# Kernel optimization log

Measured on AMD Instinct MI355X. Metric: run time of the kernel, lower is better.

The kernel has to match this reference:

```python
import jax, jax.numpy as jnp
import numpy as np

D_MODEL, D_STATE, D_CONV, EXPAND, N_HEADS = 768, 64, 4, 2, 12
D_INNER = D_MODEL * EXPAND           # 1536
HEAD_DIM = D_INNER // N_HEADS        # 128
IN_PROJ = D_INNER * 2 + N_HEADS * D_STATE * 2 + N_HEADS  # 4620
EPS = 1e-5


def setup_inputs() -> dict:
    key = jax.random.key(0)
    ks = jax.random.split(key, 8)
    s = lambda fan_in: 1.0 / np.sqrt(fan_in)
    return {
        "x": jax.random.normal(ks[0], (1, 1024, D_MODEL), dtype=jnp.float32),
        "W_in": jax.random.normal(ks[1], (IN_PROJ, D_MODEL), dtype=jnp.float32) * s(D_MODEL),
        "conv_w": jax.random.normal(ks[2], (D_INNER, D_CONV), dtype=jnp.float32) * s(D_CONV),
        "conv_b": jnp.zeros((D_INNER,), dtype=jnp.float32),
        "A_log": jnp.full((N_HEADS,), np.log(0.5), dtype=jnp.float32),
        "Dp": jnp.ones((N_HEADS,), dtype=jnp.float32),
        "dt_bias": jnp.zeros((N_HEADS,), dtype=jnp.float32),
        "W_out": jax.random.normal(ks[3], (D_MODEL, D_INNER), dtype=jnp.float32) * s(D_INNER),
        "norm_w": jnp.ones((D_INNER,), dtype=jnp.float32),
    }


def _causal_conv1d(x, w, b):
    # x: (B,L,Din), depthwise causal conv with kernel size D_CONV
    L = x.shape[1]
    xp = jnp.pad(x, ((0, 0), (D_CONV - 1, 0), (0, 0)))
    y = b
    for i in range(D_CONV):  # fixed small kernel, unrolled
        y = y + xp[:, i:i + L, :] * w[:, i]
    return y


def reference(x, W_in, conv_w, conv_b, A_log, Dp, dt_bias, W_out, norm_w):
    B_sz, L, _ = x.shape
    nh, ds, hd = N_HEADS, D_STATE, HEAD_DIM
    proj = jnp.einsum('bld,pd->blp', x, W_in)
    z = proj[:, :, :D_INNER]
    x_ssm = proj[:, :, D_INNER:2 * D_INNER]
    o = 2 * D_INNER
    Bm = proj[:, :, o:o + nh * ds].reshape(B_sz, L, nh, ds)
    Cm = proj[:, :, o + nh * ds:o + 2 * nh * ds].reshape(B_sz, L, nh, ds)
    dt_r = proj[:, :, o + 2 * nh * ds:]
    dt = jax.nn.softplus(dt_r) + dt_bias[None, None, :]          # (B,L,nh)

    x_ssm = jax.nn.silu(_causal_conv1d(x_ssm, conv_w, conv_b))
    x_ssm = x_ssm.reshape(B_sz, L, nh, hd)

    A = -jnp.exp(A_log)                                          # (nh,)
    log_decay = A[None, None, :] * dt                            # (B,L,nh)
    Phi = jnp.cumsum(log_decay, axis=1)
    dB = dt[..., None] * Bm                                      # (B,L,nh,ds)
    # b: (B,L,nh,hd,ds) outer product
    b = dB[:, :, :, None, :] * x_ssm[..., None]
    max_exp = 80.0
    exp_neg_Phi = jnp.exp(jnp.minimum(-Phi, max_exp))[..., None, None]
    b_cumsum = jnp.cumsum(exp_neg_Phi * b, axis=1)
    h = jnp.exp(Phi)[..., None, None] * b_cumsum                 # (B,L,nh,hd,ds)
    y = jnp.sum(Cm[:, :, :, None, :] * h, axis=-1)               # (B,L,nh,hd)
    y = y + Dp[None, None, :, None] * x_ssm
    y = y.reshape(B_sz, L, D_INNER)

    # RMSNorm then gate
    rms = jax.lax.rsqrt(jnp.mean(y * y, axis=-1, keepdims=True) + EPS)
    y = y * rms * norm_w
    y = y * jax.nn.silu(z)
    return jnp.einsum('bli,di->bld', y, W_out)
```

## Files before the change

### kernel.cpp

```cpp
#include <hip/hip_runtime.h>
#include <cmath>

#define LSEQ   1024
#define NPROJ  4620
#define NPADW  4736
#define DINNER 1536
#define NH     12
#define HDIM   128
#define OFF_Z  0
#define OFF_X  1536
#define OFF_B  3072
#define OFF_C  3840
#define OFF_DT 4608

typedef unsigned short u16;
typedef unsigned int u32;
typedef short bf16x8 __attribute__((ext_vector_type(8)));
typedef float f32x4 __attribute__((ext_vector_type(4)));

__device__ inline u16 f2b(float f) {
  unsigned u = __float_as_uint(f);
  return (u16)((u + 0x7fffu + ((u >> 16) & 1u)) >> 16);
}
__device__ inline float b2f(u16 h) { return __uint_as_float(((unsigned)h) << 16); }
__device__ inline u32 pk2(float a, float b) { return (u32)f2b(a) | ((u32)f2b(b) << 16); }

__device__ inline void gll16(const void* g, void* l) {
  __builtin_amdgcn_global_load_lds((const __attribute__((address_space(1))) void*)g,
                                   (__attribute__((address_space(3))) void*)l, 16, 0, 0);
}

#define S0N 196608
#define S1N 909312
#define S1V 887040
#define S2N 294912
__global__ __launch_bounds__(256) void ksplit_all(const float* __restrict__ x,
    const float* __restrict__ Wi, const float* __restrict__ Wo,
    u16* __restrict__ Ah, u16* __restrict__ Wh, u16* __restrict__ Woh) {
  int i = blockIdx.x * 256 + threadIdx.x;
  const float* src; u16* hi; int j, valid;
  if (i < S0N)            { src = x;  hi = Ah;  j = i;              valid = S0N; }
  else if (i < S0N + S1N) { src = Wi; hi = Wh;  j = i - S0N;        valid = S1V; }
  else                    { src = Wo; hi = Woh; j = i - S0N - S1N;  valid = S2N; }
  float4 v = (j < valid) ? ((const float4*)src)[j] : make_float4(0.f, 0.f, 0.f, 0.f);
  ((uint2*)hi)[j] = make_uint2(pk2(v.x, v.y), pk2(v.z, v.w));
}

template<int BM, int BN, int MAP, bool NG>
__global__ __launch_bounds__(256) void gemm1(const u16* __restrict__ Ah,
    const u16* __restrict__ Wh, float* __restrict__ C,
    int lda, int ldw, int Ksl, int Nreal, int ldc) {
  constexpr int PLA = BM * 64;
  constexpr int IA = BM / 8, IW = BN / 8, ITOT = IA + IW;
  constexpr int FRn = BN / 32;
  __shared__ u16 lds[PLA + BN * 64];
  const int tid = threadIdx.x;
  const int l = tid & 63, w = tid >> 6;
  const int wm = w >> 1, wn = w & 1;
  const int kg = l >> 4, li = l & 15;

  int b = blockIdx.x, m0, n0, koff;
  float* Cp = C;
  if (MAP == 0) {
    int xcd = b & 7, idx = b >> 3;
    m0 = (idx & 15) * 64;
    n0 = (xcd * 5 + (idx >> 4)) * 128;
    koff = 0;
    if (NG && n0 >= NPADW) return;
  } else {
    int xcd = b & 7, idx = b >> 3;
    int gg = xcd * 6 + (idx >> 4);
    m0 = (idx & 15) * 64;
    n0 = (gg % 12) * 64;
    koff = (gg / 12) * 384;
    Cp = C + (size_t)(gg / 12) * LSEQ * ldc;
  }

  const int srcg = ((l & 7) ^ (l >> 3)) * 8;
  auto stage = [&](int t) {
    const int k0 = koff + t * 64;
    for (int q = w; q < ITOT; q += 4) {
      const u16* gb; int r0b, ldk, dst;
      if (q < IA) { gb = Ah; r0b = m0 + 8 * q;        dst = 8 * q * 64;              ldk = lda; }
      else        { gb = Wh; r0b = n0 + 8 * (q - IA); dst = PLA + 8 * (q - IA) * 64; ldk = ldw; }
      gll16(gb + (size_t)(r0b + (l >> 3)) * ldk + k0 + srcg, &lds[dst]);
    }
  };
  auto rd = [&](int region, int row, int ks) -> bf16x8 {
    return *(const bf16x8*)&lds[region + row * 64 + (((ks * 4 + kg) ^ (row & 7)) << 3)];
  };

  f32x4 acc[2][FRn];
#pragma unroll
  for (int m = 0; m < 2; ++m)
#pragma unroll
    for (int n = 0; n < FRn; ++n) acc[m][n] = (f32x4){0.f, 0.f, 0.f, 0.f};

  const int NT = Ksl / 64;
  stage(0);
  asm volatile("s_waitcnt vmcnt(0)" ::: "memory");
  __syncthreads();
  for (int t = 0; t < NT; ++t) {
    bf16x8 af[2][2], wf[FRn][2];
#pragma unroll
    for (int ks = 0; ks < 2; ++ks) {
#pragma unroll
      for (int m = 0; m < 2; ++m)
        af[m][ks] = rd(0, wm * 32 + m * 16 + li, ks);
#pragma unroll
      for (int n = 0; n < FRn; ++n)
        wf[n][ks] = rd(PLA, wn * (BN / 2) + n * 16 + li, ks);
    }
    __syncthreads();
    if (t + 1 < NT) stage(t + 1);
#pragma unroll
    for (int ks = 0; ks < 2; ++ks)
#pragma unroll
      for (int m = 0; m < 2; ++m)
#pragma unroll
        for (int n = 0; n < FRn; ++n)
          acc[m][n] = __builtin_amdgcn_mfma_f32_16x16x32_bf16(af[m][ks], wf[n][ks], acc[m][n], 0, 0, 0);
    if (t + 1 < NT) {
      asm volatile("s_waitcnt vmcnt(0)" ::: "memory");
      __syncthreads();
    }
  }
#pragma unroll
  for (int m = 0; m < 2; ++m) {
    int rbase = m0 + wm * 32 + m * 16 + kg * 4;
#pragma unroll
    for (int n = 0; n < FRn; ++n) {
      int col = n0 + wn * (BN / 2) + n * 16 + li;
      if (!NG || col < Nreal) {
#pragma unroll
        for (int r = 0; r < 4; ++r)
          Cp[(size_t)(rbase + r) * ldc + col] = acc[m][n][r];
      }
    }
  }
}

__global__ __launch_bounds__(256) void addk(const float* __restrict__ P,
    float* __restrict__ out) {
  const int S = LSEQ * 768 / 4;
  int i = blockIdx.x * 256 + threadIdx.x;
  float4 a = ((const float4*)P)[i];
  float4 b = ((const float4*)P)[i + S];
  float4 c = ((const float4*)P)[i + 2 * S];
  float4 d = ((const float4*)P)[i + 3 * S];
  ((float4*)out)[i] = make_float4(a.x + b.x + c.x + d.x, a.y + b.y + c.y + d.y,
                                  a.z + b.z + c.z + d.z, a.w + b.w + c.w + d.w);
}

__global__ __launch_bounds__(256) void dtphi(const float* __restrict__ proj,
    const float* __restrict__ A_log, const float* __restrict__ dt_bias,
    float* __restrict__ Phi, float* __restrict__ dts) {
  int h = blockIdx.x, tid = threadIdx.x;
  float Ac = -expf(A_log[h]);
  float bb = dt_bias[h];
  float v[4], s = 0.f;
#pragma unroll
  for (int u = 0; u < 4; ++u) {
    int t = tid * 4 + u;
    float xr = proj[(size_t)t * NPROJ + OFF_DT + h];
    float sp = (xr > 20.f) ? xr : log1pf(expf(xr));
    v[u] = sp + bb;
    s += v[u];
  }
  int lane = tid & 63, wv = tid >> 6;
  float ps = s;
#pragma unroll
  for (int d = 1; d < 64; d <<= 1) {
    float o = __shfl_up(ps, d);
    if (lane >= d) ps += o;
  }
  __shared__ float wsum[4];
  if (lane == 63) wsum[wv] = ps;
  __syncthreads();
  float off = 0.f;
  for (int w = 0; w < wv; ++w) off += wsum[w];
  float run = off + ps - s;
#pragma unroll
  for (int u = 0; u < 4; ++u) {
    int t = tid * 4 + u;
    run += v[u];
    Phi[t * NH + h] = Ac * run;
    dts[t * NH + h] = v[u];
  }
}

__global__ __launch_bounds__(256) void conv_state(const float* __restrict__ proj,
    const float* __restrict__ cw, const float* __restrict__ cb,
    const float* __restrict__ Phi, const float* __restrict__ dts,
    u16* __restrict__ xactT, float* __restrict__ SlocF) {
  const int k = blockIdx.x, h = blockIdx.y, tid = threadIdx.x;
  const int l = tid & 63, w = tid >> 6, kg = l >> 4, li = l & 15;
  __shared__ u16 Bw[64 * 64];
  __shared__ u16 Xt[128 * 64];
  __shared__ float wS[64];
  const int s0 = k * 64;
  if (tid < 64) {
    float pe = Phi[(s0 + 63) * NH + h];
    float p  = Phi[(s0 + tid) * NH + h];
    wS[tid] = expf(pe + fminf(-p, 80.f)) * dts[(s0 + tid) * NH + h];
  }
  __syncthreads();
#pragma unroll
  for (int u = 0; u < 4; ++u) {
    int idx = tid + u * 256, s = idx >> 4, q = (idx & 15) * 4;
    float4 v = *(const float4*)(proj + (size_t)(s0 + s) * NPROJ + OFF_B + h * 64 + q);
    float ws_ = wS[s];
    float vv[4] = {v.x, v.y, v.z, v.w};
#pragma unroll
    for (int j = 0; j < 4; ++j) {
      int d = q + j;
      Bw[d * 64 + (((s >> 3) ^ (d & 7)) << 3) + (s & 7)] = f2b(vv[j] * ws_);
    }
  }
  {
    int c = tid & 127, th = tid >> 7;
    int cg = h * HDIM + c;
    float w0 = cw[cg * 4], w1 = cw[cg * 4 + 1], w2 = cw[cg * 4 + 2], w3 = cw[cg * 4 + 3];
    float bias = cb[cg];
    int tb = s0 + th * 32;
    auto P = [&](int t) { return (t >= 0) ? proj[(size_t)t * NPROJ + OFF_X + cg] : 0.f; };
    float x0 = P(tb - 3), x1 = P(tb - 2), x2 = P(tb - 1);
    u32 pkb[16];
    float prev = 0.f;
#pragma unroll
    for (int i = 0; i < 32; ++i) {
      float x3 = P(tb + i);
      float a = bias;
      a = fmaf(x0, w0, a); a = fmaf(x1, w1, a); a = fmaf(x2, w2, a); a = fmaf(x3, w3, a);
      float sv = a / (1.f + expf(-a));
      if (i & 1) pkb[i >> 1] = pk2(prev, sv); else prev = sv;
      x0 = x1; x1 = x2; x2 = x3;
    }
#pragma unroll
    for (int g = 0; g < 4; ++g) {
      int sg = th * 4 + g;
      *(uint4*)&Xt[c * 64 + ((sg ^ (c & 7)) << 3)] =
          make_uint4(pkb[g * 4], pkb[g * 4 + 1], pkb[g * 4 + 2], pkb[g * 4 + 3]);
    }
    size_t xo = ((size_t)(k * NH + h) * 128 + c) * 64 + th * 32;
#pragma unroll
    for (int g = 0; g < 4; ++g)
      *(uint4*)(xactT + xo + g * 8) =
          make_uint4(pkb[g * 4], pkb[g * 4 + 1], pkb[g * 4 + 2], pkb[g * 4 + 3]);
  }
  __syncthreads();
  const int wm = w >> 1, wn = w & 1;
  auto rd = [&](const u16* reg, int row, int ks) -> bf16x8 {
    return *(const bf16x8*)&reg[row * 64 + (((ks * 4 + kg) ^ (row & 7)) << 3)];
  };
  f32x4 acc[4][2];
#pragma unroll
  for (int m = 0; m < 4; ++m)
#pragma unroll
    for (int n = 0; n < 2; ++n) acc[m][n] = (f32x4){0.f, 0.f, 0.f, 0.f};
#pragma unroll
  for (int ks = 0; ks < 2; ++ks) {
    bf16x8 xf[4], bf[2];
#pragma unroll
    for (int m = 0; m < 4; ++m) xf[m] = rd(Xt, wm * 64 + m * 16 + li, ks);
#pragma unroll
    for (int n = 0; n < 2; ++n) bf[n] = rd(Bw, wn * 32 + n * 16 + li, ks);
#pragma unroll
    for (int m = 0; m < 4; ++m)
#pragma unroll
      for (int n = 0; n < 2; ++n)
        acc[m][n] = __builtin_amdgcn_mfma_f32_16x16x32_bf16(xf[m], bf[n], acc[m][n], 0, 0, 0);
  }
  float* dst = SlocF + ((size_t)(k * NH + h) << 13);
#pragma unroll
  for (int m = 0; m < 4; ++m)
#pragma unroll
    for (int n = 0; n < 2; ++n)
#pragma unroll
      for (int r = 0; r < 4; ++r) {
        int c = wm * 64 + m * 16 + kg * 4 + r;
        int d = wn * 32 + n * 16 + li;
        dst[c * 64 + d] = acc[m][n][r];
      }
}

__global__ __launch_bounds__(256) void chunk_scan(const float* __restrict__ SlocF,
    u16* __restrict__ SlocT, const float* __restrict__ Phi) {
  int b = blockIdx.x;
  int h = b >> 5;
  int e = (b & 31) * 256 + threadIdx.x;
  float run = SlocF[((size_t)h << 13) + e];
  SlocT[((size_t)h << 13) + e] = f2b(run);
#pragma unroll
  for (int k = 1; k < 16; ++k) {
    float lam = expf(Phi[(k * 64 + 63) * NH + h] - Phi[(k * 64 - 1) * NH + h]);
    size_t o = ((size_t)(k * NH + h) << 13) + e;
    run = fmaf(lam, run, SlocF[o]);
    SlocT[o] = f2b(run);
  }
}

__global__ __launch_bounds__(256) void ssm_out(const float* __restrict__ proj,
    const u16* __restrict__ xactT, const float* __restrict__ Phi,
    const float* __restrict__ dts, const float* __restrict__ Dp,
    const u16* __restrict__ SlocT, u16* __restrict__ ybuf) {
  const int k = blockIdx.x, h = blockIdx.y, zh = blockIdx.z, tid = threadIdx.x;
  const int l = tid & 63, w = tid >> 6, kg = l >> 4, li = l & 15;
  const int wm = w >> 1, wn = w & 1;
  __shared__ u16 Cs[4096], Bs[4096], Ps[4096], Xs[4096], Ss[4096];
  __shared__ float phiT[64], eSs[64], dSs[64], eTs[64];
  const int t0 = k * 64;
  const int srcg = ((l & 7) ^ (l >> 3)) * 8;
  {
    const u16* xsrc = xactT + ((size_t)(k * NH + h) * 128 + zh * 64) * 64;
#pragma unroll
    for (int j = 0; j < 2; ++j) {
      int rb = w * 16 + j * 8;
      gll16(xsrc + (size_t)(rb + (l >> 3)) * 64 + srcg, &Xs[rb * 64]);
    }
    if (k > 0) {
      const u16* ssrc = SlocT + (((size_t)((k - 1) * NH + h)) << 13) + (size_t)(zh * 64) * 64;
#pragma unroll
      for (int j = 0; j < 2; ++j) {
        int rb = w * 16 + j * 8;
        gll16(ssrc + (size_t)(rb + (l >> 3)) * 64 + srcg, &Ss[rb * 64]);
      }
    }
  }
#pragma unroll
  for (int u = 0; u < 4; ++u) {
    int idx = tid + u * 256, i = idx >> 4, q = (idx & 15) * 4;
    int aoff = i * 64 + (((q >> 3) ^ (i & 7)) << 3) + (q & 4);
    float4 cv = *(const float4*)(proj + (size_t)(t0 + i) * NPROJ + OFF_C + h * 64 + q);
    float4 bv = *(const float4*)(proj + (size_t)(t0 + i) * NPROJ + OFF_B + h * 64 + q);
    *(uint2*)&Cs[aoff] = make_uint2(pk2(cv.x, cv.y), pk2(cv.z, cv.w));
    *(uint2*)&Bs[aoff] = make_uint2(pk2(bv.x, bv.y), pk2(bv.z, bv.w));
  }
  if (tid < 64) {
    float p = Phi[(t0 + tid) * NH + h];
    phiT[tid] = p;
    eSs[tid] = fminf(-p, 80.f);
    dSs[tid] = dts[(t0 + tid) * NH + h];
    eTs[tid] = (k > 0) ? expf(p - Phi[(t0 - 1) * NH + h]) : 0.f;
  }
  __syncthreads();
  auto rd = [&](const u16* reg, int row, int ks) -> bf16x8 {
    return *(const bf16x8*)&reg[row * 64 + (((ks * 4 + kg) ^ (row & 7)) << 3)];
  };
  bf16x8 Cf[2][2];
  f32x4 accS[2][2];
#pragma unroll
  for (int m = 0; m < 2; ++m)
#pragma unroll
    for (int n = 0; n < 2; ++n) accS[m][n] = (f32x4){0.f, 0.f, 0.f, 0.f};
#pragma unroll
  for (int ks = 0; ks < 2; ++ks) {
    bf16x8 Bf[2];
#pragma unroll
    for (int m = 0; m < 2; ++m) Cf[m][ks] = rd(Cs, wm * 32 + m * 16 + li, ks);
#pragma unroll
    for (int n = 0; n < 2; ++n) Bf[n] = rd(Bs, wn * 32 + n * 16 + li, ks);
#pragma unroll
    for (int m = 0; m < 2; ++m)
#pragma unroll
      for (int n = 0; n < 2; ++n)
        accS[m][n] = __builtin_amdgcn_mfma_f32_16x16x32_bf16(Cf[m][ks], Bf[n], accS[m][n], 0, 0, 0);
  }
#pragma unroll
  for (int m = 0; m < 2; ++m)
#pragma unroll
    for (int n = 0; n < 2; ++n)
#pragma unroll
      for (int r = 0; r < 4; ++r) {
        int t = wm * 32 + m * 16 + kg * 4 + r;
        int s = wn * 32 + n * 16 + li;
        float f = (s <= t) ? expf(phiT[t] + eSs[s]) * dSs[s] : 0.f;
        Ps[t * 64 + (((s >> 3) ^ (t & 7)) << 3) + (s & 7)] = f2b(accS[m][n][r] * f);
      }
  __syncthreads();
  f32x4 accY[2][2], acc2[2][2];
#pragma unroll
  for (int m = 0; m < 2; ++m)
#pragma unroll
    for (int n = 0; n < 2; ++n) {
      accY[m][n] = (f32x4){0.f, 0.f, 0.f, 0.f};
      acc2[m][n] = (f32x4){0.f, 0.f, 0.f, 0.f};
    }
#pragma unroll
  for (int ks = 0; ks < 2; ++ks) {
    bf16x8 Pf[2], Xf[2];
#pragma unroll
    for (int m = 0; m < 2; ++m) Pf[m] = rd(Ps, wm * 32 + m * 16 + li, ks);
#pragma unroll
    for (int n = 0; n < 2; ++n) Xf[n] = rd(Xs, wn * 32 + n * 16 + li, ks);
#pragma unroll
    for (int m = 0; m < 2; ++m)
#pragma unroll
      for (int n = 0; n < 2; ++n)
        accY[m][n] = __builtin_amdgcn_mfma_f32_16x16x32_bf16(Pf[m], Xf[n], accY[m][n], 0, 0, 0);
    if (k > 0) {
      bf16x8 Sf[2];
#pragma unroll
      for (int n = 0; n < 2; ++n) Sf[n] = rd(Ss, wn * 32 + n * 16 + li, ks);
#pragma unroll
      for (int m = 0; m < 2; ++m)
#pragma unroll
        for (int n = 0; n < 2; ++n)
          acc2[m][n] = __builtin_amdgcn_mfma_f32_16x16x32_bf16(Cf[m][ks], Sf[n], acc2[m][n], 0, 0, 0);
    }
  }
  float dp = Dp[h];
#pragma unroll
  for (int m = 0; m < 2; ++m)
#pragma unroll
    for (int n = 0; n < 2; ++n)
#pragma unroll
      for (int r = 0; r < 4; ++r) {
        int t = wm * 32 + m * 16 + kg * 4 + r;
        int c = wn * 32 + n * 16 + li;
        float xv = b2f(Xs[c * 64 + (((t >> 3) ^ (c & 7)) << 3) + (t & 7)]);
        float val = accY[m][n][r] + eTs[t] * acc2[m][n][r] + dp * xv;
        ybuf[(size_t)(t0 + t) * DINNER + h * HDIM + zh * 64 + c] = f2b(val);
      }
}

__global__ __launch_bounds__(256) void norm_gate(const u16* __restrict__ y,
    const float* __restrict__ proj, const float* __restrict__ nw,
    u16* __restrict__ yh) {
  int t = blockIdx.x, tid = threadIdx.x;
  float v[6], ss = 0.f;
#pragma unroll
  for (int k = 0; k < 6; ++k) {
    v[k] = b2f(y[(size_t)t * DINNER + tid + k * 256]);
    ss = fmaf(v[k], v[k], ss);
  }
#pragma unroll
  for (int d = 1; d < 64; d <<= 1) ss += __shfl_xor(ss, d);
  __shared__ float wsum[4];
  int wv = tid >> 6;
  if ((tid & 63) == 0) wsum[wv] = ss;
  __syncthreads();
  float tot = wsum[0] + wsum[1] + wsum[2] + wsum[3];
  float rms = rsqrtf(tot / 1536.f + 1e-5f);
#pragma unroll
  for (int k = 0; k < 6; ++k) {
    int c = tid + k * 256;
    float z = proj[(size_t)t * NPROJ + OFF_Z + c];
    float sz = z / (1.f + expf(-z));
    yh[(size_t)t * DINNER + c] = f2b(v[k] * rms * nw[c] * sz);
  }
}

extern "C" void kernel_launch(void* const* d_in, const int* in_sizes, int n_in,
                              void* d_out, int out_size, void* d_ws, size_t ws_size,
                              hipStream_t stream) {
  const float* x       = (const float*)d_in[0];
  const float* W_in    = (const float*)d_in[1];
  const float* conv_w  = (const float*)d_in[2];
  const float* conv_b  = (const float*)d_in[3];
  const float* A_log   = (const float*)d_in[4];
  const float* Dp      = (const float*)d_in[5];
  const float* dt_bias = (const float*)d_in[6];
  const float* W_out   = (const float*)d_in[7];
  const float* norm_w  = (const float*)d_in[8];
  float* out = (float*)d_out;

  char* base = (char*)d_ws;
  size_t o = 0;
  auto alloc = [&](size_t bytes) { char* r = base + o; o += (bytes + 255) & ~(size_t)255; return r; };
  float* proj  = (float*)alloc((size_t)LSEQ * NPROJ * 4);
  u16*   ybuf  = (u16*)alloc((size_t)LSEQ * DINNER * 2);
  float* Phi   = (float*)alloc((size_t)LSEQ * NH * 4);
  float* dtsb  = (float*)alloc((size_t)LSEQ * NH * 4);
  float* SlocF = (float*)alloc((size_t)16 * NH * 8192 * 4);
  u16*   SlocT = (u16*)alloc((size_t)16 * NH * 8192 * 2);
  u16*   xactT = (u16*)alloc((size_t)16 * NH * 128 * 64 * 2);
  u16* Ah  = (u16*)alloc((size_t)LSEQ * 768 * 2);
  u16* Wh  = (u16*)alloc((size_t)NPADW * 768 * 2);
  u16* Woh = (u16*)alloc((size_t)768 * DINNER * 2);
  u16* Yh  = (u16*)alloc((size_t)LSEQ * DINNER * 2);
  float* Pp = proj;

  ksplit_all<<<dim3((S0N + S1N + S2N) / 256), 256, 0, stream>>>(
      x, W_in, W_out, Ah, Wh, Woh);
  gemm1<64, 128, 0, true><<<dim3(640), 256, 0, stream>>>(
      Ah, Wh, proj, 768, 768, 768, NPROJ, NPROJ);
  dtphi<<<dim3(NH), 256, 0, stream>>>(proj, A_log, dt_bias, Phi, dtsb);
  conv_state<<<dim3(16, NH), 256, 0, stream>>>(proj, conv_w, conv_b, Phi, dtsb, xactT, SlocF);
  chunk_scan<<<dim3(NH * 32), 256, 0, stream>>>(SlocF, SlocT, Phi);
  ssm_out<<<dim3(16, NH, 2), 256, 0, stream>>>(proj, xactT, Phi, dtsb, Dp, SlocT, ybuf);
  norm_gate<<<dim3(LSEQ), 256, 0, stream>>>(ybuf, proj, norm_w, Yh);
  gemm1<64, 64, 1, false><<<dim3(768), 256, 0, stream>>>(
      Yh, Woh, Pp, 1536, 1536, 384, 768, 768);
  addk<<<dim3(LSEQ * 768 / 4 / 256), 256, 0, stream>>>(Pp, out);
}
```

Measured before the change: 72.25 us.

## Fuse mid-pipeline SSM kernels into one persistent kernel with grid barriers

Replaces the five middle kernels (dt/Phi scan, conv+chunk state, chunk scan, SSM output, norm+gate) with a single 192-block kernel. The stages are separated by atomic-counter grid barriers, and the counters are reset by the first conversion kernel. The aim is to remove four launch gaps and their tail effects between small kernels. In exchange it relies on all 192 blocks being co-resident, and it shrinks parallelism in stages that used more blocks before (ssm_out had 384, norm_gate had 1024). The output-GEMM partials also move from the proj buffer to a separate Pp allocation.

```diff
diff --git a/kernel.cpp b/kernel.cpp
--- a/kernel.cpp
+++ b/kernel.cpp
@@ -30,13 +30,26 @@
                                    (__attribute__((address_space(3))) void*)l, 16, 0, 0);
 }
 
+__device__ inline void gbar(int* ctr, int idx) {
+  __syncthreads();
+  if (threadIdx.x == 0) {
+    __threadfence();
+    atomicAdd(&ctr[idx], 1);
+    while (atomicAdd(&ctr[idx], 0) < 192) __builtin_amdgcn_s_sleep(2);
+    __threadfence();
+  }
+  __syncthreads();
+}
+
 #define S0N 196608
 #define S1N 909312
 #define S1V 887040
 #define S2N 294912
 __global__ __launch_bounds__(256) void ksplit_all(const float* __restrict__ x,
     const float* __restrict__ Wi, const float* __restrict__ Wo,
-    u16* __restrict__ Ah, u16* __restrict__ Wh, u16* __restrict__ Woh) {
+    u16* __restrict__ Ah, u16* __restrict__ Wh, u16* __restrict__ Woh,
+    int* __restrict__ ctr) {
+  if (blockIdx.x == 0 && threadIdx.x < 8) ctr[threadIdx.x] = 0;
   int i = blockIdx.x * 256 + threadIdx.x;
   const float* src; u16* hi; int j, valid;
   if (i < S0N)            { src = x;  hi = Ah;  j = i;              valid = S0N; }
@@ -51,7 +64,7 @@
     const u16* __restrict__ Wh, float* __restrict__ C,
     int lda, int ldw, int Ksl, int Nreal, int ldc) {
   constexpr int PLA = BM * 64;
-  constexpr int IA = BM / 8, IW = BN / 8, ITOT = IA + IW;
+  constexpr int IA = BM / 8, ITOT = IA + BN / 8;
   constexpr int FRn = BN / 32;
   __shared__ u16 lds[PLA + BN * 64];
   const int tid = threadIdx.x;
@@ -152,302 +165,342 @@
                                   a.z + b.z + c.z + d.z, a.w + b.w + c.w + d.w);
 }
 
-__global__ __launch_bounds__(256) void dtphi(const float* __restrict__ proj,
+__global__ __launch_bounds__(256) void mid_all(const float* __restrict__ proj,
+    const float* __restrict__ cw, const float* __restrict__ cb,
     const float* __restrict__ A_log, const float* __restrict__ dt_bias,
-    float* __restrict__ Phi, float* __restrict__ dts) {
-  int h = blockIdx.x, tid = threadIdx.x;
-  float Ac = -expf(A_log[h]);
-  float bb = dt_bias[h];
-  float v[4], s = 0.f;
-#pragma unroll
-  for (int u = 0; u < 4; ++u) {
-    int t = tid * 4 + u;
-    float xr = proj[(size_t)t * NPROJ + OFF_DT + h];
-    float sp = (xr > 20.f) ? xr : log1pf(expf(xr));
-    v[u] = sp + bb;
-    s += v[u];
-  }
-  int lane = tid & 63, wv = tid >> 6;
-  float ps = s;
-#pragma unroll
-  for (int d = 1; d < 64; d <<= 1) {
-    float o = __shfl_up(ps, d);
-    if (lane >= d) ps += o;
-  }
+    const float* __restrict__ Dp, const float* __restrict__ nw,
+    float* __restrict__ Phi, float* __restrict__ dts,
+    u16* __restrict__ xactT, float* __restrict__ SlocF, u16* __restrict__ SlocT,
+    u16* __restrict__ ybuf, u16* __restrict__ Yh, int* __restrict__ ctr) {
+  const int bid = blockIdx.x, tid = threadIdx.x;
+  const int l = tid & 63, w = tid >> 6, kg = l >> 4, li = l & 15;
+  __shared__ u16 Bw[4096];
+  __shared__ u16 Xt[8192];
+  __shared__ u16 Cs[4096], Bs[4096], Ps[4096], Xs[4096], Ss[4096];
+  __shared__ float wS[64];
+  __shared__ float phiT[64], eSs[64], dSs[64], eTs[64];
   __shared__ float wsum[4];
-  if (lane == 63) wsum[wv] = ps;
-  __syncthreads();
-  float off = 0.f;
-  for (int w = 0; w < wv; ++w) off += wsum[w];
-  float run = off + ps - s;
-#pragma unroll
-  for (int u = 0; u < 4; ++u) {
-    int t = tid * 4 + u;
-    run += v[u];
-    Phi[t * NH + h] = Ac * run;
-    dts[t * NH + h] = v[u];
-  }
-}
-
-__global__ __launch_bounds__(256) void conv_state(const float* __restrict__ proj,
-    const float* __restrict__ cw, const float* __restrict__ cb,
-    const float* __restrict__ Phi, const float* __restrict__ dts,
-    u16* __restrict__ xactT, float* __restrict__ SlocF) {
-  const int k = blockIdx.x, h = blockIdx.y, tid = threadIdx.x;
-  const int l = tid & 63, w = tid >> 6, kg = l >> 4, li = l & 15;
-  __shared__ u16 Bw[64 * 64];
-  __shared__ u16 Xt[128 * 64];
-  __shared__ float wS[64];
-  const int s0 = k * 64;
-  if (tid < 64) {
-    float pe = Phi[(s0 + 63) * NH + h];
-    float p  = Phi[(s0 + tid) * NH + h];
-    wS[tid] = expf(pe + fminf(-p, 80.f)) * dts[(s0 + tid) * NH + h];
-  }
-  __syncthreads();
-#pragma unroll
-  for (int u = 0; u < 4; ++u) {
-    int idx = tid + u * 256, s = idx >> 4, q = (idx & 15) * 4;
-    float4 v = *(const float4*)(proj + (size_t)(s0 + s) * NPROJ + OFF_B + h * 64 + q);
-    float ws_ = wS[s];
-    float vv[4] = {v.x, v.y, v.z, v.w};
-#pragma unroll
-    for (int j = 0; j < 4; ++j) {
-      int d = q + j;
-      Bw[d * 64 + (((s >> 3) ^ (d & 7)) << 3) + (s & 7)] = f2b(vv[j] * ws_);
-    }
-  }
+
+  if (bid < NH) {
+    const int h = bid;
+    float Ac = -expf(A_log[h]);
+    float bb = dt_bias[h];
+    float v[4], s = 0.f;
+#pragma unroll
+    for (int u = 0; u < 4; ++u) {
+      int t = tid * 4 + u;
+      float xr = proj[(size_t)t * NPROJ + OFF_DT + h];
+      float sp = (xr > 20.f) ? xr : log1pf(expf(xr));
+      v[u] = sp + bb;
+      s += v[u];
+    }
+    int lane = tid & 63, wv = tid >> 6;
+    float ps = s;
+#pragma unroll
+    for (int d = 1; d < 64; d <<= 1) {
+      float o = __shfl_up(ps, d);
+      if (lane >= d) ps += o;
+    }
+    if (lane == 63) wsum[wv] = ps;
+    __syncthreads();
+    float off = 0.f;
+    for (int q = 0; q < wv; ++q) off += wsum[q];
+    float run = off + ps - s;
+#pragma unroll
+    for (int u = 0; u < 4; ++u) {
+      int t = tid * 4 + u;
+      run += v[u];
+      Phi[t * NH + h] = Ac * run;
+      dts[t * NH + h] = v[u];
+    }
+  }
+  gbar(ctr, 0);
+
   {
-    int c = tid & 127, th = tid >> 7;
-    int cg = h * HDIM + c;
-    float w0 = cw[cg * 4], w1 = cw[cg * 4 + 1], w2 = cw[cg * 4 + 2], w3 = cw[cg * 4 + 3];
-    float bias = cb[cg];
-    int tb = s0 + th * 32;
-    auto P = [&](int t) { return (t >= 0) ? proj[(size_t)t * NPROJ + OFF_X + cg] : 0.f; };
-    float x0 = P(tb - 3), x1 = P(tb - 2), x2 = P(tb - 1);
-    u32 pkb[16];
-    float prev = 0.f;
-#pragma unroll
-    for (int i = 0; i < 32; ++i) {
-      float x3 = P(tb + i);
-      float a = bias;
-      a = fmaf(x0, w0, a); a = fmaf(x1, w1, a); a = fmaf(x2, w2, a); a = fmaf(x3, w3, a);
-      float sv = a / (1.f + expf(-a));
-      if (i & 1) pkb[i >> 1] = pk2(prev, sv); else prev = sv;
-      x0 = x1; x1 = x2; x2 = x3;
-    }
-#pragma unroll
-    for (int g = 0; g < 4; ++g) {
-      int sg = th * 4 + g;
-      *(uint4*)&Xt[c * 64 + ((sg ^ (c & 7)) << 3)] =
-          make_uint4(pkb[g * 4], pkb[g * 4 + 1], pkb[g * 4 + 2], pkb[g * 4 + 3]);
-    }
-    size_t xo = ((size_t)(k * NH + h) * 128 + c) * 64 + th * 32;
-#pragma unroll
-    for (int g = 0; g < 4; ++g)
-      *(uint4*)(xactT + xo + g * 8) =
-          make_uint4(pkb[g * 4], pkb[g * 4 + 1], pkb[g * 4 + 2], pkb[g * 4 + 3]);
-  }
-  __syncthreads();
-  const int wm = w >> 1, wn = w & 1;
-  auto rd = [&](const u16* reg, int row, int ks) -> bf16x8 {
-    return *(const bf16x8*)&reg[row * 64 + (((ks * 4 + kg) ^ (row & 7)) << 3)];
-  };
-  f32x4 acc[4][2];
-#pragma unroll
-  for (int m = 0; m < 4; ++m)
-#pragma unroll
-    for (int n = 0; n < 2; ++n) acc[m][n] = (f32x4){0.f, 0.f, 0.f, 0.f};
-#pragma unroll
-  for (int ks = 0; ks < 2; ++ks) {
-    bf16x8 xf[4], bf[2];
-#pragma unroll
-    for (int m = 0; m < 4; ++m) xf[m] = rd(Xt, wm * 64 + m * 16 + li, ks);
-#pragma unroll
-    for (int n = 0; n < 2; ++n) bf[n] = rd(Bw, wn * 32 + n * 16 + li, ks);
+    const int k = bid & 15, h = bid >> 4;
+    const int s0 = k * 64;
+    if (tid < 64) {
+      float pe = Phi[(s0 + 63) * NH + h];
+      float p  = Phi[(s0 + tid) * NH + h];
+      wS[tid] = expf(pe + fminf(-p, 80.f)) * dts[(s0 + tid) * NH + h];
+    }
+    __syncthreads();
+#pragma unroll
+    for (int u = 0; u < 4; ++u) {
+      int idx = tid + u * 256, s = idx >> 4, q = (idx & 15) * 4;
+      float4 v = *(const float4*)(proj + (size_t)(s0 + s) * NPROJ + OFF_B + h * 64 + q);
+      float ws_ = wS[s];
+      float vv[4] = {v.x, v.y, v.z, v.w};
+#pragma unroll
+      for (int j = 0; j < 4; ++j) {
+        int d = q + j;
+        Bw[d * 64 + (((s >> 3) ^ (d & 7)) << 3) + (s & 7)] = f2b(vv[j] * ws_);
+      }
+    }
+    {
+      int c = tid & 127, th = tid >> 7;
+      int cg = h * HDIM + c;
+      float w0 = cw[cg * 4], w1 = cw[cg * 4 + 1], w2 = cw[cg * 4 + 2], w3 = cw[cg * 4 + 3];
+      float bias = cb[cg];
+      int tb = s0 + th * 32;
+      auto P = [&](int t) { return (t >= 0) ? proj[(size_t)t * NPROJ + OFF_X + cg] : 0.f; };
+      float x0 = P(tb - 3), x1 = P(tb - 2), x2 = P(tb - 1);
+      u32 pkb[16];
+      float prev = 0.f;
+#pragma unroll
+      for (int i = 0; i < 32; ++i) {
+        float x3 = P(tb + i);
+        float a = bias;
+        a = fmaf(x0, w0, a); a = fmaf(x1, w1, a); a = fmaf(x2, w2, a); a = fmaf(x3, w3, a);
+        float sv = a / (1.f + expf(-a));
+        if (i & 1) pkb[i >> 1] = pk2(prev, sv); else prev = sv;
+        x0 = x1; x1 = x2; x2 = x3;
+      }
+#pragma unroll
+      for (int g = 0; g < 4; ++g) {
+        int sg = th * 4 + g;
+        *(uint4*)&Xt[c * 64 + ((sg ^ (c & 7)) << 3)] =
+            make_uint4(pkb[g * 4], pkb[g * 4 + 1], pkb[g * 4 + 2], pkb[g * 4 + 3]);
+      }
+      size_t xo = ((size_t)(k * NH + h) * 128 + c) * 64 + th * 32;
+#pragma unroll
+      for (int g = 0; g < 4; ++g)
+        *(uint4*)(xactT + xo + g * 8) =
+            make_uint4(pkb[g * 4], pkb[g * 4 + 1], pkb[g * 4 + 2], pkb[g * 4 + 3]);
+    }
+    __syncthreads();
+    const int wm = w >> 1, wn = w & 1;
+    auto rd2 = [&](const u16* reg, int row, int ks) -> bf16x8 {
+      return *(const bf16x8*)&reg[row * 64 + (((ks * 4 + kg) ^ (row & 7)) << 3)];
+    };
+    f32x4 acc[4][2];
 #pragma unroll
     for (int m = 0; m < 4; ++m)
 #pragma unroll
+      for (int n = 0; n < 2; ++n) acc[m][n] = (f32x4){0.f, 0.f, 0.f, 0.f};
+#pragma unroll
+    for (int ks = 0; ks < 2; ++ks) {
+      bf16x8 xf[4], bf[2];
+#pragma unroll
+      for (int m = 0; m < 4; ++m) xf[m] = rd2(Xt, wm * 64 + m * 16 + li, ks);
+#pragma unroll
+      for (int n = 0; n < 2; ++n) bf[n] = rd2(Bw, wn * 32 + n * 16 + li, ks);
+#pragma unroll
+      for (int m = 0; m < 4; ++m)
+#pragma unroll
+        for (int n = 0; n < 2; ++n)
+          acc[m][n] = __builtin_amdgcn_mfma_f32_16x16x32_bf16(xf[m], bf[n], acc[m][n], 0, 0, 0);
+    }
+    float* dst = SlocF + (((size_t)(k * NH + h)) << 13);
+#pragma unroll
+    for (int m = 0; m < 4; ++m)
+#pragma unroll
       for (int n = 0; n < 2; ++n)
-        acc[m][n] = __builtin_amdgcn_mfma_f32_16x16x32_bf16(xf[m], bf[n], acc[m][n], 0, 0, 0);
-  }
-  float* dst = SlocF + ((size_t)(k * NH + h) << 13);
-#pragma unroll
-  for (int m = 0; m < 4; ++m)
-#pragma unroll
-    for (int n = 0; n < 2; ++n)
-#pragma unroll
-      for (int r = 0; r < 4; ++r) {
-        int c = wm * 64 + m * 16 + kg * 4 + r;
-        int d = wn * 32 + n * 16 + li;
-        dst[c * 64 + d] = acc[m][n][r];
-      }
-}
-
-__global__ __launch_bounds__(256) void chunk_scan(const float* __restrict__ SlocF,
-    u16* __restrict__ SlocT, const float* __restrict__ Phi) {
-  int b = blockIdx.x;
-  int h = b >> 5;
-  int e = (b & 31) * 256 + threadIdx.x;
-  float run = SlocF[((size_t)h << 13) + e];
-  SlocT[((size_t)h << 13) + e] = f2b(run);
-#pragma unroll
-  for (int k = 1; k < 16; ++k) {
-    float lam = expf(Phi[(k * 64 + 63) * NH + h] - Phi[(k * 64 - 1) * NH + h]);
-    size_t o = ((size_t)(k * NH + h) << 13) + e;
-    run = fmaf(lam, run, SlocF[o]);
-    SlocT[o] = f2b(run);
-  }
-}
-
-__global__ __launch_bounds__(256) void ssm_out(const float* __restrict__ proj,
-    const u16* __restrict__ xactT, const float* __restrict__ Phi,
-    const float* __restrict__ dts, const float* __restrict__ Dp,
-    const u16* __restrict__ SlocT, u16* __restrict__ ybuf) {
-  const int k = blockIdx.x, h = blockIdx.y, zh = blockIdx.z, tid = threadIdx.x;
-  const int l = tid & 63, w = tid >> 6, kg = l >> 4, li = l & 15;
-  const int wm = w >> 1, wn = w & 1;
-  __shared__ u16 Cs[4096], Bs[4096], Ps[4096], Xs[4096], Ss[4096];
-  __shared__ float phiT[64], eSs[64], dSs[64], eTs[64];
-  const int t0 = k * 64;
-  const int srcg = ((l & 7) ^ (l >> 3)) * 8;
+#pragma unroll
+        for (int r = 0; r < 4; ++r) {
+          int c = wm * 64 + m * 16 + kg * 4 + r;
+          int d = wn * 32 + n * 16 + li;
+          dst[c * 64 + d] = acc[m][n][r];
+        }
+  }
+  gbar(ctr, 1);
+
   {
-    const u16* xsrc = xactT + ((size_t)(k * NH + h) * 128 + zh * 64) * 64;
+    int vb = bid * 2;
+    int h3 = vb >> 5;
+    int e0 = (vb & 31) * 256 + tid;
+    float r0 = SlocF[((size_t)h3 << 13) + e0];
+    float r1 = SlocF[((size_t)h3 << 13) + e0 + 256];
+    SlocT[((size_t)h3 << 13) + e0] = f2b(r0);
+    SlocT[((size_t)h3 << 13) + e0 + 256] = f2b(r1);
+#pragma unroll
+    for (int k3 = 1; k3 < 16; ++k3) {
+      float lam = expf(Phi[(k3 * 64 + 63) * NH + h3] - Phi[(k3 * 64 - 1) * NH + h3]);
+      size_t o = ((size_t)(k3 * NH + h3) << 13) + e0;
+      r0 = fmaf(lam, r0, SlocF[o]);
+      r1 = fmaf(lam, r1, SlocF[o + 256]);
+      SlocT[o] = f2b(r0);
+      SlocT[o + 256] = f2b(r1);
+    }
+  }
+  gbar(ctr, 2);
+
+  {
+    const int k = bid & 15, h = bid >> 4;
+    const int wm = w >> 1, wn = w & 1;
+    const int t0 = k * 64;
+    const int srcg = ((l & 7) ^ (l >> 3)) * 8;
+    const size_t xbase = ((size_t)(k * NH + h) * 128) * 64;
+    const u16* ssrc = SlocT + (((size_t)((k > 0 ? k - 1 : 0) * NH + h) * 128) << 6);
+#pragma unroll
+    for (int u = 0; u < 4; ++u) {
+      int idx = tid + u * 256, i = idx >> 4, q = (idx & 15) * 4;
+      int aoff = i * 64 + (((q >> 3) ^ (i & 7)) << 3) + (q & 4);
+      float4 cv = *(const float4*)(proj + (size_t)(t0 + i) * NPROJ + OFF_C + h * 64 + q);
+      float4 bv = *(const float4*)(proj + (size_t)(t0 + i) * NPROJ + OFF_B + h * 64 + q);
+      *(uint2*)&Cs[aoff] = make_uint2(pk2(cv.x, cv.y), pk2(cv.z, cv.w));
+      *(uint2*)&Bs[aoff] = make_uint2(pk2(bv.x, bv.y), pk2(bv.z, bv.w));
+    }
 #pragma unroll
     for (int j = 0; j < 2; ++j) {
       int rb = w * 16 + j * 8;
-      gll16(xsrc + (size_t)(rb + (l >> 3)) * 64 + srcg, &Xs[rb * 64]);
+      gll16(xactT + xbase + (size_t)(rb + (l >> 3)) * 64 + srcg, &Xs[rb * 64]);
     }
     if (k > 0) {
-      const u16* ssrc = SlocT + (((size_t)((k - 1) * NH + h)) << 13) + (size_t)(zh * 64) * 64;
 #pragma unroll
       for (int j = 0; j < 2; ++j) {
         int rb = w * 16 + j * 8;
         gll16(ssrc + (size_t)(rb + (l >> 3)) * 64 + srcg, &Ss[rb * 64]);
       }
     }
-  }
-#pragma unroll
-  for (int u = 0; u < 4; ++u) {
-    int idx = tid + u * 256, i = idx >> 4, q = (idx & 15) * 4;
-    int aoff = i * 64 + (((q >> 3) ^ (i & 7)) << 3) + (q & 4);
-    float4 cv = *(const float4*)(proj + (size_t)(t0 + i) * NPROJ + OFF_C + h * 64 + q);
-    float4 bv = *(const float4*)(proj + (size_t)(t0 + i) * NPROJ + OFF_B + h * 64 + q);
-    *(uint2*)&Cs[aoff] = make_uint2(pk2(cv.x, cv.y), pk2(cv.z, cv.w));
-    *(uint2*)&Bs[aoff] = make_uint2(pk2(bv.x, bv.y), pk2(bv.z, bv.w));
-  }
-  if (tid < 64) {
-    float p = Phi[(t0 + tid) * NH + h];
-    phiT[tid] = p;
-    eSs[tid] = fminf(-p, 80.f);
-    dSs[tid] = dts[(t0 + tid) * NH + h];
-    eTs[tid] = (k > 0) ? expf(p - Phi[(t0 - 1) * NH + h]) : 0.f;
-  }
-  __syncthreads();
-  auto rd = [&](const u16* reg, int row, int ks) -> bf16x8 {
-    return *(const bf16x8*)&reg[row * 64 + (((ks * 4 + kg) ^ (row & 7)) << 3)];
-  };
-  bf16x8 Cf[2][2];
-  f32x4 accS[2][2];
-#pragma unroll
-  for (int m = 0; m < 2; ++m)
-#pragma unroll
-    for (int n = 0; n < 2; ++n) accS[m][n] = (f32x4){0.f, 0.f, 0.f, 0.f};
-#pragma unroll
-  for (int ks = 0; ks < 2; ++ks) {
-    bf16x8 Bf[2];
-#pragma unroll
-    for (int m = 0; m < 2; ++m) Cf[m][ks] = rd(Cs, wm * 32 + m * 16 + li, ks);
-#pragma unroll
-    for (int n = 0; n < 2; ++n) Bf[n] = rd(Bs, wn * 32 + n * 16 + li, ks);
+    if (tid < 64) {
+      float p = Phi[(t0 + tid) * NH + h];
+      phiT[tid] = p;
+      eSs[tid] = fminf(-p, 80.f);
+      dSs[tid] = dts[(t0 + tid) * NH + h];
+      eTs[tid] = (k > 0) ? expf(p - Phi[(t0 - 1) * NH + h]) : 0.f;
+    }
+    __syncthreads();
+    auto rd4 = [&](const u16* reg, int row, int ks) -> bf16x8 {
+      return *(const bf16x8*)&reg[row * 64 + (((ks * 4 + kg) ^ (row & 7)) << 3)];
+    };
+    bf16x8 Cf[2][2];
+    f32x4 accS[2][2];
 #pragma unroll
     for (int m = 0; m < 2; ++m)
 #pragma unroll
+      for (int n = 0; n < 2; ++n) accS[m][n] = (f32x4){0.f, 0.f, 0.f, 0.f};
+#pragma unroll
+    for (int ks = 0; ks < 2; ++ks) {
+      bf16x8 Bf[2];
+#pragma unroll
+      for (int m = 0; m < 2; ++m) Cf[m][ks] = rd4(Cs, wm * 32 + m * 16 + li, ks);
+#pragma unroll
+      for (int n = 0; n < 2; ++n) Bf[n] = rd4(Bs, wn * 32 + n * 16 + li, ks);
+#pragma unroll
+      for (int m = 0; m < 2; ++m)
+#pragma unroll
+        for (int n = 0; n < 2; ++n)
+          accS[m][n] = __builtin_amdgcn_mfma_f32_16x16x32_bf16(Cf[m][ks], Bf[n], accS[m][n], 0, 0, 0);
+    }
+#pragma unroll
+    for (int m = 0; m < 2; ++m)
+#pragma unroll
       for (int n = 0; n < 2; ++n)
-        accS[m][n] = __builtin_amdgcn_mfma_f32_16x16x32_bf16(Cf[m][ks], Bf[n], accS[m][n], 0, 0, 0);
-  }
-#pragma unroll
-  for (int m = 0; m < 2; ++m)
-#pragma unroll
-    for (int n = 0; n < 2; ++n)
-#pragma unroll
-      for (int r = 0; r < 4; ++r) {
-        int t = wm * 32 + m * 16 + kg * 4 + r;
-        int s = wn * 32 + n * 16 + li;
-        float f = (s <= t) ? expf(phiT[t] + eSs[s]) * dSs[s] : 0.f;
-        Ps[t * 64 + (((s >> 3) ^ (t & 7)) << 3) + (s & 7)] = f2b(accS[m][n][r] * f);
-      }
-  __syncthreads();
-  f32x4 accY[2][2], acc2[2][2];
-#pragma unroll
-  for (int m = 0; m < 2; ++m)
-#pragma unroll
-    for (int n = 0; n < 2; ++n) {
-      accY[m][n] = (f32x4){0.f, 0.f, 0.f, 0.f};
-      acc2[m][n] = (f32x4){0.f, 0.f, 0.f, 0.f};
-    }
-#pragma unroll
-  for (int ks = 0; ks < 2; ++ks) {
-    bf16x8 Pf[2], Xf[2];
-#pragma unroll
-    for (int m = 0; m < 2; ++m) Pf[m] = rd(Ps, wm * 32 + m * 16 + li, ks);
-#pragma unroll
-    for (int n = 0; n < 2; ++n) Xf[n] = rd(Xs, wn * 32 + n * 16 + li, ks);
-#pragma unroll
-    for (int m = 0; m < 2; ++m)
-#pragma unroll
-      for (int n = 0; n < 2; ++n)
-        accY[m][n] = __builtin_amdgcn_mfma_f32_16x16x32_bf16(Pf[m], Xf[n], accY[m][n], 0, 0, 0);
-    if (k > 0) {
-      bf16x8 Sf[2];
-#pragma unroll
-      for (int n = 0; n < 2; ++n) Sf[n] = rd(Ss, wn * 32 + n * 16 + li, ks);
+#pragma unroll
+        for (int r = 0; r < 4; ++r) {
+          int t = wm * 32 + m * 16 + kg * 4 + r;
+          int s = wn * 32 + n * 16 + li;
+          float f = (s <= t) ? expf(phiT[t] + eSs[s]) * dSs[s] : 0.f;
+          Ps[t * 64 + (((s >> 3) ^ (t & 7)) << 3) + (s & 7)] = f2b(accS[m][n][r] * f);
+        }
+    __syncthreads();
+    float dp = Dp[h];
+    for (int zh = 0; zh < 2; ++zh) {
+      f32x4 accY[2][2], acc2[2][2];
 #pragma unroll
       for (int m = 0; m < 2; ++m)
 #pragma unroll
+        for (int n = 0; n < 2; ++n) {
+          accY[m][n] = (f32x4){0.f, 0.f, 0.f, 0.f};
+          acc2[m][n] = (f32x4){0.f, 0.f, 0.f, 0.f};
+        }
+#pragma unroll
+      for (int ks = 0; ks < 2; ++ks) {
+        bf16x8 Pf[2], Xf[2];
+#pragma unroll
+        for (int m = 0; m < 2; ++m) Pf[m] = rd4(Ps, wm * 32 + m * 16 + li, ks);
+#pragma unroll
+        for (int n = 0; n < 2; ++n) Xf[n] = rd4(Xs, wn * 32 + n * 16 + li, ks);
+#pragma unroll
+        for (int m = 0; m < 2; ++m)
+#pragma unroll
+          for (int n = 0; n < 2; ++n)
+            accY[m][n] = __builtin_amdgcn_mfma_f32_16x16x32_bf16(Pf[m], Xf[n], accY[m][n], 0, 0, 0);
+        if (k > 0) {
+          bf16x8 Sf[2];
+#pragma unroll
+          for (int n = 0; n < 2; ++n) Sf[n] = rd4(Ss, wn * 32 + n * 16 + li, ks);
+#pragma unroll
+          for (int m = 0; m < 2; ++m)
+#pragma unroll
+            for (int n = 0; n < 2; ++n)
+              acc2[m][n] = __builtin_amdgcn_mfma_f32_16x16x32_bf16(Cf[m][ks], Sf[n], acc2[m][n], 0, 0, 0);
+        }
+      }
+#pragma unroll
+      for (int m = 0; m < 2; ++m)
+#pragma unroll
         for (int n = 0; n < 2; ++n)
-          acc2[m][n] = __builtin_amdgcn_mfma_f32_16x16x32_bf16(Cf[m][ks], Sf[n], acc2[m][n], 0, 0, 0);
-    }
-  }
-  float dp = Dp[h];
-#pragma unroll
-  for (int m = 0; m < 2; ++m)
-#pragma unroll
-    for (int n = 0; n < 2; ++n)
-#pragma unroll
-      for (int r = 0; r < 4; ++r) {
-        int t = wm * 32 + m * 16 + kg * 4 + r;
-        int c = wn * 32 + n * 16 + li;
-        float xv = b2f(Xs[c * 64 + (((t >> 3) ^ (c & 7)) << 3) + (t & 7)]);
-        float val = accY[m][n][r] + eTs[t] * acc2[m][n][r] + dp * xv;
-        ybuf[(size_t)(t0 + t) * DINNER + h * HDIM + zh * 64 + c] = f2b(val);
-      }
-}
-
-__global__ __launch_bounds__(256) void norm_gate(const u16* __restrict__ y,
-    const float* __restrict__ proj, const float* __restrict__ nw,
-    u16* __restrict__ yh) {
-  int t = blockIdx.x, tid = threadIdx.x;
-  float v[6], ss = 0.f;
-#pragma unroll
-  for (int k = 0; k < 6; ++k) {
-    v[k] = b2f(y[(size_t)t * DINNER + tid + k * 256]);
-    ss = fmaf(v[k], v[k], ss);
-  }
-#pragma unroll
-  for (int d = 1; d < 64; d <<= 1) ss += __shfl_xor(ss, d);
-  __shared__ float wsum[4];
-  int wv = tid >> 6;
-  if ((tid & 63) == 0) wsum[wv] = ss;
-  __syncthreads();
-  float tot = wsum[0] + wsum[1] + wsum[2] + wsum[3];
-  float rms = rsqrtf(tot / 1536.f + 1e-5f);
-#pragma unroll
-  for (int k = 0; k < 6; ++k) {
-    int c = tid + k * 256;
-    float z = proj[(size_t)t * NPROJ + OFF_Z + c];
-    float sz = z / (1.f + expf(-z));
-    yh[(size_t)t * DINNER + c] = f2b(v[k] * rms * nw[c] * sz);
+#pragma unroll
+          for (int r = 0; r < 4; ++r) {
+            int t = wm * 32 + m * 16 + kg * 4 + r;
+            int c = wn * 32 + n * 16 + li;
+            float xv = b2f(Xs[c * 64 + (((t >> 3) ^ (c & 7)) << 3) + (t & 7)]);
+            float val = accY[m][n][r] + eTs[t] * acc2[m][n][r] + dp * xv;
+            ybuf[(size_t)(t0 + t) * DINNER + h * HDIM + zh * 64 + c] = f2b(val);
+          }
+      if (zh == 0) {
+        __syncthreads();
+#pragma unroll
+        for (int j = 0; j < 2; ++j) {
+          int rb = w * 16 + j * 8;
+          gll16(xactT + xbase + (size_t)(64 + rb + (l >> 3)) * 64 + srcg, &Xs[rb * 64]);
+        }
+        if (k > 0) {
+#pragma unroll
+          for (int j = 0; j < 2; ++j) {
+            int rb = w * 16 + j * 8;
+            gll16(ssrc + (size_t)(64 + rb + (l >> 3)) * 64 + srcg, &Ss[rb * 64]);
+          }
+        }
+        __syncthreads();
+      }
+    }
+  }
+  gbar(ctr, 3);
+
+  {
+    float nwv[6];
+    {
+      const float* nr = nw + tid * 6;
+      float2 a = *(const float2*)nr, b = *(const float2*)(nr + 2), c = *(const float2*)(nr + 4);
+      nwv[0] = a.x; nwv[1] = a.y; nwv[2] = b.x; nwv[3] = b.y; nwv[4] = c.x; nwv[5] = c.y;
+    }
+    for (int t = bid; t < LSEQ; t += 192) {
+      const u16* yr = ybuf + (size_t)t * DINNER + tid * 6;
+      u32 y0 = *(const u32*)yr, y1 = *(const u32*)(yr + 2), y2 = *(const u32*)(yr + 4);
+      float v[6] = {b2f((u16)y0), b2f((u16)(y0 >> 16)), b2f((u16)y1),
+                    b2f((u16)(y1 >> 16)), b2f((u16)y2), b2f((u16)(y2 >> 16))};
+      float ss = 0.f;
+#pragma unroll
+      for (int j = 0; j < 6; ++j) ss = fmaf(v[j], v[j], ss);
+#pragma unroll
+      for (int d = 1; d < 64; d <<= 1) ss += __shfl_xor(ss, d);
+      if ((tid & 63) == 0) wsum[tid >> 6] = ss;
+      __syncthreads();
+      float tot = wsum[0] + wsum[1] + wsum[2] + wsum[3];
+      float rms = rsqrtf(tot / 1536.f + 1e-5f);
+      const float* zr = proj + (size_t)t * NPROJ + OFF_Z + tid * 6;
+      float2 z0 = *(const float2*)zr, z1 = *(const float2*)(zr + 2), z2 = *(const float2*)(zr + 4);
+      float zz[6] = {z0.x, z0.y, z1.x, z1.y, z2.x, z2.y};
+      u32 o[3];
+      float r01 = 0, r23 = 0;
+#pragma unroll
+      for (int j = 0; j < 6; ++j) {
+        float sz = zz[j] / (1.f + expf(-zz[j]));
+        float val = v[j] * rms * nwv[j] * sz;
+        if (j == 0) r01 = val;
+        else if (j == 1) o[0] = pk2(r01, val);
+        else if (j == 2) r23 = val;
+        else if (j == 3) o[1] = pk2(r23, val);
+        else if (j == 4) r01 = val;
+        else o[2] = pk2(r01, val);
+      }
+      u16* dst = Yh + (size_t)t * DINNER + tid * 6;
+      *(u32*)dst = o[0]; *(u32*)(dst + 2) = o[1]; *(u32*)(dst + 4) = o[2];
+      __syncthreads();
+    }
   }
 }
 
@@ -469,27 +522,26 @@
   size_t o = 0;
   auto alloc = [&](size_t bytes) { char* r = base + o; o += (bytes + 255) & ~(size_t)255; return r; };
   float* proj  = (float*)alloc((size_t)LSEQ * NPROJ * 4);
-  u16*   ybuf  = (u16*)alloc((size_t)LSEQ * DINNER * 2);
   float* Phi   = (float*)alloc((size_t)LSEQ * NH * 4);
-  float* dtsb  = (float*)alloc((size_t)LSEQ * NH * 4);
+  float* dts   = (float*)alloc((size_t)LSEQ * NH * 4);
   float* SlocF = (float*)alloc((size_t)16 * NH * 8192 * 4);
   u16*   SlocT = (u16*)alloc((size_t)16 * NH * 8192 * 2);
-  u16*   xactT = (u16*)alloc((size_t)16 * NH * 128 * 64 * 2);
-  u16* Ah  = (u16*)alloc((size_t)LSEQ * 768 * 2);
-  u16* Wh  = (u16*)alloc((size_t)NPADW * 768 * 2);
-  u16* Woh = (u16*)alloc((size_t)768 * DINNER * 2);
-  u16* Yh  = (u16*)alloc((size_t)LSEQ * DINNER * 2);
-  float* Pp = proj;
+  u16*   xactT = (u16*)alloc((size_t)16 * NH * 8192 * 2);
+  u16*   ybuf  = (u16*)alloc((size_t)LSEQ * DINNER * 2);
+  u16*   Ah    = (u16*)alloc((size_t)LSEQ * 768 * 2);
+  u16*   Wh    = (u16*)alloc((size_t)NPADW * 768 * 2);
+  u16*   Woh   = (u16*)alloc((size_t)768 * DINNER * 2);
+  u16*   Yh    = (u16*)alloc((size_t)LSEQ * DINNER * 2);
+  float* Pp    = (float*)alloc((size_t)4 * LSEQ * 768 * 4);
+  int*   ctr   = (int*)alloc(256);
 
   ksplit_all<<<dim3((S0N + S1N + S2N) / 256), 256, 0, stream>>>(
-      x, W_in, W_out, Ah, Wh, Woh);
+      x, W_in, W_out, Ah, Wh, Woh, ctr);
   gemm1<64, 128, 0, true><<<dim3(640), 256, 0, stream>>>(
       Ah, Wh, proj, 768, 768, 768, NPROJ, NPROJ);
-  dtphi<<<dim3(NH), 256, 0, stream>>>(proj, A_log, dt_bias, Phi, dtsb);
-  conv_state<<<dim3(16, NH), 256, 0, stream>>>(proj, conv_w, conv_b, Phi, dtsb, xactT, SlocF);
-  chunk_scan<<<dim3(NH * 32), 256, 0, stream>>>(SlocF, SlocT, Phi);
-  ssm_out<<<dim3(16, NH, 2), 256, 0, stream>>>(proj, xactT, Phi, dtsb, Dp, SlocT, ybuf);
-  norm_gate<<<dim3(LSEQ), 256, 0, stream>>>(ybuf, proj, norm_w, Yh);
+  mid_all<<<dim3(192), 256, 0, stream>>>(
+      proj, conv_w, conv_b, A_log, dt_bias, Dp, norm_w,
+      Phi, dts, xactT, SlocF, SlocT, ybuf, Yh, ctr);
   gemm1<64, 64, 1, false><<<dim3(768), 256, 0, stream>>>(
       Yh, Woh, Pp, 1536, 1536, 384, 768, 768);
   addk<<<dim3(LSEQ * 768 / 4 / 256), 256, 0, stream>>>(Pp, out);
```

After: 133.2 us. 1.84x slower.
